# Kernel optimization log

Measured on AMD Instinct MI355X. Metric: run time of the kernel, lower is better.

Reference implementation:

```python
import jax, jax.numpy as jnp
import numpy as np
import math

B, S, D, H = 2, 1024, 4096, 32
HD = D // H          # head_dim = 128
P = 10               # prompt_len
THETA = 500000.0     # rope_theta


def _rope(t, cos, sin):
    # t: [b, s, h, hd]; pairs (2i, 2i+1) form complex numbers as in view_as_complex
    tr = t[..., 0::2]
    ti = t[..., 1::2]
    c = cos[None, :, None, :]
    s = sin[None, :, None, :]
    out = jnp.stack([tr * c - ti * s, tr * s + ti * c], axis=-1)  # [b,s,h,hd/2,2]
    return out.reshape(t.shape)


def setup_inputs() -> dict:
    key = jax.random.key(0)
    ks = jax.random.split(key, 8)
    sc = 0.02
    x = jax.random.normal(ks[0], (B, S, D), jnp.float32)
    wq = jax.random.normal(ks[1], (D, D), jnp.float32) * sc
    wk = jax.random.normal(ks[2], (D, D), jnp.float32) * sc
    wv = jax.random.normal(ks[3], (D, D), jnp.float32) * sc
    wo = jax.random.normal(ks[4], (D, D), jnp.float32) * sc
    prompt = jax.random.normal(ks[5], (P, D), jnp.float32)
    prompt_gate = jax.random.normal(ks[6], (1, H, 1, 1), jnp.float32) * 0.1
    # RoPE tables (real/imag of freqs_cis)
    inv = 1.0 / (THETA ** (jnp.arange(0, HD, 2, dtype=jnp.float32) / HD))  # [HD/2]
    ang = jnp.outer(jnp.arange(S, dtype=jnp.float32), inv)                 # [S, HD/2]
    freqs_cos = jnp.cos(ang)
    freqs_sin = jnp.sin(ang)
    # causal additive mask
    mask = jnp.triu(jnp.full((S, S), -1e9, jnp.float32), 1)[None, None]
    type_weight = jax.random.uniform(ks[7], (B, S, 1), jnp.float32)
    return dict(x=x, wq=wq, wk=wk, wv=wv, wo=wo, prompt=prompt,
                prompt_gate=prompt_gate, freqs_cos=freqs_cos,
                freqs_sin=freqs_sin, mask=mask, type_weight=type_weight,
                start_pos=0)


def reference(x, wq, wk, wv, wo, prompt, prompt_gate, freqs_cos, freqs_sin,
              mask, type_weight, start_pos):
    # training-mode forward: start_pos == 0, keys/values = current tokens
    scale = 1.0 / math.sqrt(HD)
    xq = (x @ wq.T).reshape(B, S, H, HD)
    xk = (x @ wk.T).reshape(B, S, H, HD)
    xv = (x @ wv.T).reshape(B, S, H, HD)
    xq = _rope(xq, freqs_cos, freqs_sin)
    xk = _rope(xk, freqs_cos, freqs_sin)
    q = xq.transpose(0, 2, 1, 3)  # [b,h,s,hd]
    k = xk.transpose(0, 2, 1, 3)
    v = xv.transpose(0, 2, 1, 3)
    scores = jnp.einsum('bhqd,bhkd->bhqk', q, k) * scale + mask
    probs = jax.nn.softmax(scores, axis=-1)
    out = jnp.einsum('bhqk,bhkd->bhqd', probs, v)  # [b,h,s,hd]
    # gated prompt injection (num_experts == 1); type_weight unused, as in source
    pk = (prompt @ wk.T).reshape(P, H, HD)
    pv = (prompt @ wv.T).reshape(P, H, HD)
    p_scores = jnp.einsum('bhqd,phd->bhqp', q, pk) * scale
    p_probs = prompt_gate * jax.nn.softmax(p_scores, axis=-1)
    p_out = jnp.einsum('bhqp,phd->bhqd', p_probs, pv)
    out = (out + p_out).transpose(0, 2, 1, 3).reshape(B, S, D)
    return out @ wo.T
```

## Files before the change

kernel.cpp:

```cpp
#include <hip/hip_runtime.h>
#include <hip/hip_bf16.h>
#include <stdint.h>

typedef __hip_bfloat16 bf16;
typedef __attribute__((ext_vector_type(8))) short short8;
typedef __attribute__((ext_vector_type(4))) float f32x4;

#define SCALE_ 0.08838834764831845f

static __device__ __forceinline__ float bf2f(short u) {
  unsigned int x = ((unsigned int)(unsigned short)u) << 16;
  return __builtin_bit_cast(float, x);
}
static __device__ __forceinline__ short f2bf(float f) {
  __hip_bfloat16 h = __float2bfloat16(f);
  return __builtin_bit_cast(short, h);
}
static __device__ __forceinline__ f32x4 mfma16(short8 a, short8 b, f32x4 c) {
  return __builtin_amdgcn_mfma_f32_16x16x32_bf16(a, b, c, 0, 0, 0);
}
static __device__ __forceinline__ void gl_lds16(const bf16* g, bf16* l) {
  __builtin_amdgcn_global_load_lds(
      (const __attribute__((address_space(1))) unsigned int*)g,
      (__attribute__((address_space(3))) unsigned int*)l, 16, 0, 0);
}

__global__ __launch_bounds__(256) void cvt6(
    const float* __restrict__ sx, const float* __restrict__ sq,
    const float* __restrict__ sk, const float* __restrict__ sv,
    const float* __restrict__ so, const float* __restrict__ sp,
    bf16* __restrict__ dx, bf16* __restrict__ dq, bf16* __restrict__ dk,
    bf16* __restrict__ dv, bf16* __restrict__ d4, bf16* __restrict__ dp)
{
  int b = blockIdx.x;
  const float* s; bf16* d; int off;
  if (b < 4096)       { s = sx; d = dx; off = b; }
  else if (b < 12288) { s = sq; d = dq; off = b - 4096; }
  else if (b < 20480) { s = sk; d = dk; off = b - 12288; }
  else if (b < 28672) { s = sv; d = dv; off = b - 20480; }
  else if (b < 36864) { s = so; d = d4; off = b - 28672; }
  else                { s = sp; d = dp; off = b - 36864; }
  long base = (long)off * 2048 + threadIdx.x * 8;
  f32x4 a = *(const f32x4*)(s + base);
  f32x4 c = *(const f32x4*)(s + base + 4);
  short8 o;
#pragma unroll
  for (int j = 0; j < 4; j++) { o[j] = f2bf(a[j]); o[4 + j] = f2bf(c[j]); }
  *(short8*)(d + base) = o;
}

__global__ __launch_bounds__(512, 2) void gemm_bt(
    const bf16* __restrict__ A, const bf16* __restrict__ A2,
    const bf16* __restrict__ B0, const bf16* __restrict__ B1, const bf16* __restrict__ B2w,
    bf16* __restrict__ C0, bf16* __restrict__ C1, bf16* __restrict__ C2,
    bf16* __restrict__ P1, bf16* __restrict__ P2,
    float* __restrict__ CF,
    int M1, int Mtot)
{
  __shared__ char lds[131072];
  const int tid = threadIdx.x, w = tid >> 6, l = tid & 63;
  const int lr = l & 15, lg = l >> 4;
  const int wm = w >> 2, wn = w & 3;
  const int z = blockIdx.z;
  const bf16* Bw = (z == 0) ? B0 : ((z == 1) ? B1 : B2w);
  bf16* C  = (z == 0) ? C0 : ((z == 1) ? C1 : C2);
  bf16* Cp = (z == 0) ? (bf16*)0 : ((z == 1) ? P1 : P2);

  const int cpx = gridDim.x >> 3, orig = blockIdx.x;
  const int wg = (orig & 7) * cpx + (orig >> 3);
  const long m0 = (long)(wg >> 4) * 256;
  const long n0 = (long)(wg & 15) * 256;

  const int r0 = ((tid >> 3) << 1) | ((tid >> 2) & 1);
  const int c0 = (tid & 3) ^ ((tid >> 3) & 3);
  const bf16 *pa0, *pa1;
  {
    long mx = (long)(Mtot - M1) - 1;
    long g0 = m0 + r0, g1 = m0 + r0 + 128;
    const bf16 *q0, *q1;
    if (g0 < M1) q0 = A + g0 * 4096;
    else { long rr = g0 - M1; if (rr > mx) rr = mx; q0 = A2 + rr * 4096; }
    if (g1 < M1) q1 = A + g1 * 4096;
    else { long rr = g1 - M1; if (rr > mx) rr = mx; q1 = A2 + rr * 4096; }
    pa0 = q0 + c0 * 8;
    pa1 = q1 + c0 * 8;
  }
  const bf16* pb0 = Bw + (n0 + r0) * 4096 + c0 * 8;
  const bf16* pb1 = pb0 + (long)128 * 4096;

  const int ro  = (lr >> 1) * 128 + (((lr & 1) * 4) + (lg ^ ((lr >> 1) & 3))) * 16;
  const int aro = wm * 8192 + ro;
  const int bro = wn * 4096 + ro;

  f32x4 acc[8][4];
#pragma unroll
  for (int i = 0; i < 8; i++)
#pragma unroll
    for (int j = 0; j < 4; j++) acc[i][j] = (f32x4){0.f, 0.f, 0.f, 0.f};

  short8 af[4], bf[4];

#define STG(PSB_, J_, P0_, P1_, KE_)                                         \
  {                                                                          \
    bf16* d_ = (bf16*)(lds + (PSB_) + (J_) * 16384) + tid * 8;               \
    gl_lds16((P0_) + (KE_), d_);                                             \
    gl_lds16((P1_) + (KE_), d_ + 4096);                                      \
  }

#define PHASE(VMS_, PRB_, AU_, BU_, MO_, LB_, STGC_)                         \
  {                                                                          \
    asm volatile("s_waitcnt vmcnt(" VMS_ ")" ::: "memory");                  \
    __builtin_amdgcn_s_barrier();                                            \
    __builtin_amdgcn_sched_barrier(0);                                       \
    STGC_                                                                    \
    const char* ab_ = lds + (PRB_) + (AU_) + aro;                            \
    _Pragma("unroll") for (int mi = 0; mi < 4; mi++)                         \
      af[mi] = *(const short8*)(ab_ + ((MO_) + mi) * 1024);                  \
    if (LB_) {                                                               \
      const char* bb_ = lds + (PRB_) + (BU_) + bro;                          \
      _Pragma("unroll") for (int ni = 0; ni < 4; ni++)                       \
        bf[ni] = *(const short8*)(bb_ + ni * 1024);                          \
    }                                                                        \
    asm volatile("s_waitcnt lgkmcnt(0)" ::: "memory");                       \
    __builtin_amdgcn_sched_barrier(0);                                       \
    __builtin_amdgcn_s_setprio(1);                                           \
    _Pragma("unroll") for (int mi = 0; mi < 4; mi++)                         \
      _Pragma("unroll") for (int ni = 0; ni < 4; ni++)                       \
        acc[(MO_) + mi][ni] = mfma16(af[mi], bf[ni], acc[(MO_) + mi][ni]);   \
    __builtin_amdgcn_s_setprio(0);                                           \
  }

#define KTILE(PRB_, PSB_, KE_)                                               \
  PHASE("4", PRB_, 0,     16384, 0, 1, STG(PSB_, 0, pa0, pa1, (KE_)))        \
  PHASE("4", PRB_, 0,     16384, 4, 0, STG(PSB_, 1, pb0, pb1, (KE_)))        \
  PHASE("4", PRB_, 32768, 49152, 0, 1, STG(PSB_, 2, pa0, pa1, (KE_) + 32))   \
  PHASE("4", PRB_, 32768, 49152, 4, 0, STG(PSB_, 3, pb0, pb1, (KE_) + 32))

#define KTILE_LAST(PRB_)                                                     \
  PHASE("4", PRB_, 0,     16384, 0, 1, )                                     \
  PHASE("4", PRB_, 0,     16384, 4, 0, )                                     \
  PHASE("0", PRB_, 32768, 49152, 0, 1, )                                     \
  PHASE("0", PRB_, 32768, 49152, 4, 0, )

  STG(0, 0, pa0, pa1, 0)
  STG(0, 1, pb0, pb1, 0)
  STG(0, 2, pa0, pa1, 32)
  STG(0, 3, pb0, pb1, 32)

  for (int kt = 0; kt < 62; kt += 2) {
    const int ke1 = (kt + 1) * 64;
    const int ke2 = (kt + 2) * 64;
    KTILE(0, 65536, ke1)
    KTILE(65536, 0, ke2)
  }
  KTILE(0, 65536, 4032)
  KTILE_LAST(65536)

#undef KTILE_LAST
#undef KTILE
#undef PHASE
#undef STG

#pragma unroll
  for (int mi = 0; mi < 8; mi++) {
#pragma unroll
    for (int ni = 0; ni < 4; ni++) {
      long col = n0 + wn * 64 + ni * 16 + lr;
      f32x4 v = acc[mi][ni];
#pragma unroll
      for (int j = 0; j < 4; j++) {
        long row = m0 + wm * 128 + mi * 16 + lg * 4 + j;
        if (CF) {
          CF[row * 4096 + col] = v[j];
        } else if (row < M1) {
          *(short*)(C + row * 4096 + col) = f2bf(v[j]);
        } else if (Cp != 0 && row < Mtot) {
          *(short*)(Cp + (row - M1) * 4096 + col) = f2bf(v[j]);
        }
      }
    }
  }
}

__global__ __launch_bounds__(256) void rope_qk(
    bf16* __restrict__ Q, bf16* __restrict__ Kb,
    const float* __restrict__ FC, const float* __restrict__ FS)
{
  const int row = blockIdx.x;
  const int s = row & 1023;
  const int t = threadIdx.x;
  bf16* base = (blockIdx.y ? Kb : Q) + (long)row * 4096 + t * 16;
  short8 v0 = *(const short8*)base;
  short8 v1 = *(const short8*)(base + 8);
  const float* cp = FC + s * 64 + (t & 7) * 8;
  const float* sp = FS + s * 64 + (t & 7) * 8;
  f32x4 c0 = *(const f32x4*)cp;
  f32x4 c1 = *(const f32x4*)(cp + 4);
  f32x4 s0 = *(const f32x4*)sp;
  f32x4 s1 = *(const f32x4*)(sp + 4);
  short8 o0, o1;
#pragma unroll
  for (int j = 0; j < 4; j++) {
    float c = c0[j], sn = s0[j];
    float e = bf2f(v0[2 * j]), od = bf2f(v0[2 * j + 1]);
    o0[2 * j] = f2bf(e * c - od * sn);
    o0[2 * j + 1] = f2bf(e * sn + od * c);
    float c2 = c1[j], sn2 = s1[j];
    float e2 = bf2f(v1[2 * j]), od2 = bf2f(v1[2 * j + 1]);
    o1[2 * j] = f2bf(e2 * c2 - od2 * sn2);
    o1[2 * j + 1] = f2bf(e2 * sn2 + od2 * c2);
  }
  *(short8*)base = o0;
  *(short8*)(base + 8) = o1;
}

__global__ __launch_bounds__(256) void transpose_v(
    const bf16* __restrict__ V, bf16* __restrict__ VT)
{
  __shared__ bf16 T[64 * 128];
  const int tid = threadIdx.x;
  const int st = blockIdx.x * 64, bh = blockIdx.y;
  const int b = bh >> 5, h = bh & 31;
  const bf16* src = V + ((long)(b * 1024 + st)) * 4096 + h * 128;
#pragma unroll
  for (int rr = 0; rr < 4; ++rr) {
    int i = tid + rr * 256;
    int s_l = i >> 4, c = i & 15;
    short8 v = *(const short8*)(src + (long)s_l * 4096 + c * 8);
    *(short8*)((char*)T + s_l * 256 + ((c ^ (s_l & 7)) * 16)) = v;
  }
  __syncthreads();
#pragma unroll
  for (int rr = 0; rr < 4; ++rr) {
    int i = tid + rr * 256;
    int d = i >> 3, cs = i & 7;
    short8 ov;
#pragma unroll
    for (int e = 0; e < 8; e++) {
      int s_l = cs * 8 + e;
      ov[e] = *(const short*)((char*)T + s_l * 256 + (((d >> 3) ^ (s_l & 7)) * 16) + (d & 7) * 2);
    }
    *(short8*)(VT + ((long)bh * 128 + d) * 1024 + st + cs * 8) = ov;
  }
}

__global__ __launch_bounds__(256) void flash_attn(
    const bf16* __restrict__ Q, const bf16* __restrict__ Kg, const bf16* __restrict__ VT,
    const bf16* __restrict__ PK, const bf16* __restrict__ PV,
    const float* __restrict__ GATE, bf16* __restrict__ O)
{
  __shared__ bf16 Kl[32 * 128];
  __shared__ bf16 Vl[128 * 32];
  __shared__ bf16 PKl[16 * 128];
  __shared__ bf16 PVl[128 * 16];
  __shared__ bf16 Pl[4][16 * 32];
  const int tid = threadIdx.x, w = tid >> 6, l = tid & 63;
  const int lg = l >> 4, lr = l & 15;
  const int qb = blockIdx.x, bh = blockIdx.y;
  const int b = bh >> 5, h = bh & 31;
  const int q0 = qb * 64 + w * 16;

  short8 qf[4];
  {
    const bf16* qp = Q + ((long)(b * 1024 + q0 + lr)) * 4096 + h * 128 + lg * 8;
#pragma unroll
    for (int c = 0; c < 4; c++) qf[c] = *(const short8*)(qp + c * 32);
  }
  {
    int rowp = tid >> 4, pc = tid & 15, lc = pc ^ (rowp & 7);
    short8 v = {0, 0, 0, 0, 0, 0, 0, 0};
    if (rowp < 10) v = *(const short8*)(PK + (long)rowp * 4096 + h * 128 + lc * 8);
    *(short8*)((char*)PKl + tid * 16) = v;
  }
  {
    int d = tid >> 1, pb = (tid & 1) * 8;
#pragma unroll
    for (int e = 0; e < 8; e++) {
      int p = pb + e;
      short v = 0;
      if (p < 10) v = __builtin_bit_cast(short, PV[(long)p * 4096 + h * 128 + d]);
      *(short*)((char*)PVl + d * 32 + (((p >> 3) ^ (d & 1)) * 16) + (p & 7) * 2) = v;
    }
  }
  const float gate = GATE[h];

  f32x4 o[8];
#pragma unroll
  for (int i = 0; i < 8; i++) o[i] = (f32x4){0.f, 0.f, 0.f, 0.f};
  float m_[4] = {-1e30f, -1e30f, -1e30f, -1e30f};
  float l_[4] = {0.f, 0.f, 0.f, 0.f};

  const int nt = (qb + 1) * 2;
  const bf16* Kbase = Kg + ((long)b * 1024) * 4096 + h * 128;
  const bf16* Vbase = VT + ((long)bh) * 128 * 1024;
  const int cb1 = w * 64, cb2 = 256 + w * 64;
  const int iA = cb1 + l, iB = cb2 + l;
  bf16* pw = &Pl[w][0];

  for (int j = 0; j < nt; ++j) {
    __syncthreads();
    {
      const bf16* gA = Kbase + (long)(j * 32 + (iA >> 4)) * 4096 + ((iA & 15) ^ ((iA >> 4) & 7)) * 8;
      const bf16* gB = Kbase + (long)(j * 32 + (iB >> 4)) * 4096 + ((iB & 15) ^ ((iB >> 4) & 7)) * 8;
      gl_lds16(gA, Kl + cb1 * 8);
      gl_lds16(gB, Kl + cb2 * 8);
      const bf16* vA = Vbase + (long)(iA >> 2) * 1024 + j * 32 + ((iA & 3) ^ ((iA >> 2) & 3)) * 8;
      const bf16* vB = Vbase + (long)(iB >> 2) * 1024 + j * 32 + ((iB & 3) ^ ((iB >> 2) & 3)) * 8;
      gl_lds16(vA, Vl + cb1 * 8);
      gl_lds16(vB, Vl + cb2 * 8);
    }
    __syncthreads();

    f32x4 s[2];
#pragma unroll
    for (int ns = 0; ns < 2; ns++) {
      f32x4 a = (f32x4){0.f, 0.f, 0.f, 0.f};
      int krow = ns * 16 + lr;
      const char* kp = (const char*)Kl + krow * 256;
      int sw = krow & 7;
#pragma unroll
      for (int c = 0; c < 4; c++) {
        short8 kf = *(const short8*)(kp + (((c * 4 + lg) ^ sw) * 16));
        a = mfma16(qf[c], kf, a);
      }
      int key = j * 32 + krow;
#pragma unroll
      for (int r = 0; r < 4; r++) {
        int qr = q0 + lg * 4 + r;
        s[ns][r] = a[r] * SCALE_ + ((key <= qr) ? 0.0f : -1e30f);
      }
    }
    float mx[4], cor[4], sum[4];
#pragma unroll
    for (int r = 0; r < 4; r++) mx[r] = fmaxf(s[0][r], s[1][r]);
#pragma unroll
    for (int xm = 1; xm < 16; xm <<= 1)
#pragma unroll
      for (int r = 0; r < 4; r++) mx[r] = fmaxf(mx[r], __shfl_xor(mx[r], xm, 64));
#pragma unroll
    for (int r = 0; r < 4; r++) {
      float mn = fmaxf(m_[r], mx[r]);
      cor[r] = __expf(m_[r] - mn);
      m_[r] = mn;
      s[0][r] = __expf(s[0][r] - mn);
      s[1][r] = __expf(s[1][r] - mn);
      sum[r] = s[0][r] + s[1][r];
    }
#pragma unroll
    for (int xm = 1; xm < 16; xm <<= 1)
#pragma unroll
      for (int r = 0; r < 4; r++) sum[r] += __shfl_xor(sum[r], xm, 64);
#pragma unroll
    for (int r = 0; r < 4; r++) l_[r] = l_[r] * cor[r] + sum[r];
#pragma unroll
    for (int df = 0; df < 8; df++)
#pragma unroll
      for (int r = 0; r < 4; r++) o[df][r] *= cor[r];

#pragma unroll
    for (int ns = 0; ns < 2; ns++)
#pragma unroll
      for (int r = 0; r < 4; r++)
        *(short*)((char*)pw + ((lg * 4 + r) * 32 + ns * 16 + lr) * 2) = f2bf(s[ns][r]);
    asm volatile("s_waitcnt lgkmcnt(0)" ::: "memory");
    __builtin_amdgcn_sched_barrier(0);
    short8 pf = *(const short8*)(pw + lr * 32 + lg * 8);

#pragma unroll
    for (int df = 0; df < 8; df++) {
      int d = df * 16 + lr;
      short8 vf = *(const short8*)((const char*)Vl + d * 64 + ((lg ^ (d & 3)) * 16));
      o[df] = mfma16(pf, vf, o[df]);
    }
  }

  f32x4 ps;
  {
    f32x4 a = (f32x4){0.f, 0.f, 0.f, 0.f};
    const char* kp = (const char*)PKl + lr * 256;
    int sw = lr & 7;
#pragma unroll
    for (int c = 0; c < 4; c++) {
      short8 kf = *(const short8*)(kp + (((c * 4 + lg) ^ sw) * 16));
      a = mfma16(qf[c], kf, a);
    }
#pragma unroll
    for (int r = 0; r < 4; r++) ps[r] = (lr < 10) ? a[r] * SCALE_ : -1e30f;
  }
  {
    float pm[4], pss[4];
#pragma unroll
    for (int r = 0; r < 4; r++) pm[r] = ps[r];
#pragma unroll
    for (int xm = 1; xm < 16; xm <<= 1)
#pragma unroll
      for (int r = 0; r < 4; r++) pm[r] = fmaxf(pm[r], __shfl_xor(pm[r], xm, 64));
#pragma unroll
    for (int r = 0; r < 4; r++) { ps[r] = __expf(ps[r] - pm[r]); pss[r] = ps[r]; }
#pragma unroll
    for (int xm = 1; xm < 16; xm <<= 1)
#pragma unroll
      for (int r = 0; r < 4; r++) pss[r] += __shfl_xor(pss[r], xm, 64);
#pragma unroll
    for (int r = 0; r < 4; r++) ps[r] = ps[r] / pss[r];
  }
#pragma unroll
  for (int r = 0; r < 4; r++) {
    *(short*)((char*)pw + ((lg * 4 + r) * 32 + lr) * 2) = f2bf(ps[r]);
    *(short*)((char*)pw + ((lg * 4 + r) * 32 + 16 + lr) * 2) = 0;
  }
  asm volatile("s_waitcnt lgkmcnt(0)" ::: "memory");
  __builtin_amdgcn_sched_barrier(0);
  short8 pf2 = *(const short8*)(pw + lr * 32 + lg * 8);
  f32x4 po[8];
#pragma unroll
  for (int df = 0; df < 8; df++) {
    int d = df * 16 + lr;
    short8 vf = {0, 0, 0, 0, 0, 0, 0, 0};
    if (lg < 2) vf = *(const short8*)((const char*)PVl + d * 32 + ((lg ^ (d & 1)) * 16));
    po[df] = mfma16(pf2, vf, (f32x4){0.f, 0.f, 0.f, 0.f});
  }

  bf16* op = O + ((long)(b * 1024 + q0 + lg * 4)) * 4096 + h * 128 + lr;
#pragma unroll
  for (int df = 0; df < 8; df++)
#pragma unroll
    for (int r = 0; r < 4; r++) {
      float val = o[df][r] / l_[r] + gate * po[df][r];
      *(short*)(op + (long)r * 4096 + df * 16) = f2bf(val);
    }
}

extern "C" void kernel_launch(void* const* d_in, const int* in_sizes, int n_in,
                              void* d_out, int out_size, void* d_ws, size_t ws_size,
                              hipStream_t stream) {
  (void)in_sizes; (void)n_in; (void)out_size; (void)ws_size;
  const float* x      = (const float*)d_in[0];
  const float* wq     = (const float*)d_in[1];
  const float* wk     = (const float*)d_in[2];
  const float* wv     = (const float*)d_in[3];
  const float* wo     = (const float*)d_in[4];
  const float* prompt = (const float*)d_in[5];
  const float* gate   = (const float*)d_in[6];
  const float* fcos   = (const float*)d_in[7];
  const float* fsin   = (const float*)d_in[8];
  float* out = (float*)d_out;
  char* ws = (char*)d_ws;

  size_t o = 0;
  bf16* xb  = (bf16*)(ws + o); o += (size_t)8388608 * 2;
  bf16* wqb = (bf16*)(ws + o); o += (size_t)16777216 * 2;
  bf16* wkb = (bf16*)(ws + o); o += (size_t)16777216 * 2;
  bf16* wvb = (bf16*)(ws + o); o += (size_t)16777216 * 2;
  bf16* wob = (bf16*)(ws + o); o += (size_t)16777216 * 2;
  bf16* pb  = (bf16*)(ws + o); o += (size_t)40960 * 2;
  bf16* q_ws  = (bf16*)(ws + o); o += (size_t)2048 * 4096 * 2;
  bf16* k_ws  = (bf16*)(ws + o); o += (size_t)2048 * 4096 * 2;
  bf16* v_ws  = (bf16*)(ws + o); o += (size_t)2048 * 4096 * 2;
  bf16* vT_ws = (bf16*)(ws + o); o += (size_t)2048 * 4096 * 2;
  bf16* pk_ws = (bf16*)(ws + o); o += (size_t)40960 * 2;
  bf16* pv_ws = (bf16*)(ws + o); o += (size_t)40960 * 2;
  bf16* attn_ws = v_ws;

  cvt6<<<dim3(36884), 256, 0, stream>>>(x, wq, wk, wv, wo, prompt,
                                        xb, wqb, wkb, wvb, wob, pb);
  gemm_bt<<<dim3(144, 1, 3), 512, 0, stream>>>(
      xb, pb, wqb, wkb, wvb, q_ws, k_ws, v_ws, pk_ws, pv_ws, (float*)0, 2048, 2058);
  rope_qk<<<dim3(2048, 2), 256, 0, stream>>>(q_ws, k_ws, fcos, fsin);
  transpose_v<<<dim3(16, 64), 256, 0, stream>>>(v_ws, vT_ws);
  flash_attn<<<dim3(16, 64), 256, 0, stream>>>(
      q_ws, k_ws, vT_ws, pk_ws, pv_ws, gate, attn_ws);
  gemm_bt<<<dim3(128, 1, 1), 512, 0, stream>>>(
      attn_ws, (const bf16*)0, wob, wob, wob, q_ws, q_ws, q_ws,
      (bf16*)0, (bf16*)0, out, 2048, 2048);
}
```

Before: 530.5 us.

## Deepen GEMM LDS prefetch pipeline and halve barriers per k-tile

Restructures the GEMM main loop so global-to-LDS staging runs further ahead, with six sub-tiles in flight before the first compute instead of four. The eight LDS slots rotate in a new order. Barriers with vmcnt waits now happen once per two phases instead of every phase, which cuts synchronisation stalls. In exchange, each wait tolerates more outstanding loads and the slot reuse is more complex, so there is a risk of LDS read/write races if the slot ordering is wrong.

New measurement: 534.2 us. No clear change (+0.7%).

```diff
diff --git a/kernel.cpp b/kernel.cpp
--- a/kernel.cpp
+++ b/kernel.cpp
@@ -100,19 +100,27 @@
 
   short8 af[4], bf[4];
 
-#define STG(PSB_, J_, P0_, P1_, KE_)                                         \
+#define STGA(S_, KE_)                                                        \
   {                                                                          \
-    bf16* d_ = (bf16*)(lds + (PSB_) + (J_) * 16384) + tid * 8;               \
-    gl_lds16((P0_) + (KE_), d_);                                             \
-    gl_lds16((P1_) + (KE_), d_ + 4096);                                      \
-  }
-
-#define PHASE(VMS_, PRB_, AU_, BU_, MO_, LB_, STGC_)                         \
+    bf16* d_ = (bf16*)(lds + (S_) * 16384) + tid * 8;                        \
+    gl_lds16(pa0 + (KE_), d_);                                               \
+    gl_lds16(pa1 + (KE_), d_ + 4096);                                        \
+  }
+#define STGB(S_, KE_)                                                        \
   {                                                                          \
-    asm volatile("s_waitcnt vmcnt(" VMS_ ")" ::: "memory");                  \
+    bf16* d_ = (bf16*)(lds + (S_) * 16384) + tid * 8;                        \
+    gl_lds16(pb0 + (KE_), d_);                                               \
+    gl_lds16(pb1 + (KE_), d_ + 4096);                                        \
+  }
+#define SYNC(VM_)                                                            \
+  {                                                                          \
+    asm volatile("s_waitcnt vmcnt(" VM_ ")" ::: "memory");                   \
     __builtin_amdgcn_s_barrier();                                            \
     __builtin_amdgcn_sched_barrier(0);                                       \
-    STGC_                                                                    \
+  }
+#define PHASE(PRB_, AU_, BU_, MO_, LB_, STG_)                                \
+  {                                                                          \
+    STG_                                                                     \
     const char* ab_ = lds + (PRB_) + (AU_) + aro;                            \
     _Pragma("unroll") for (int mi = 0; mi < 4; mi++)                         \
       af[mi] = *(const short8*)(ab_ + ((MO_) + mi) * 1024);                  \
@@ -130,36 +138,34 @@
     __builtin_amdgcn_s_setprio(0);                                           \
   }
 
-#define KTILE(PRB_, PSB_, KE_)                                               \
-  PHASE("4", PRB_, 0,     16384, 0, 1, STG(PSB_, 0, pa0, pa1, (KE_)))        \
-  PHASE("4", PRB_, 0,     16384, 4, 0, STG(PSB_, 1, pb0, pb1, (KE_)))        \
-  PHASE("4", PRB_, 32768, 49152, 0, 1, STG(PSB_, 2, pa0, pa1, (KE_) + 32))   \
-  PHASE("4", PRB_, 32768, 49152, 4, 0, STG(PSB_, 3, pb0, pb1, (KE_) + 32))
-
-#define KTILE_LAST(PRB_)                                                     \
-  PHASE("4", PRB_, 0,     16384, 0, 1, )                                     \
-  PHASE("4", PRB_, 0,     16384, 4, 0, )                                     \
-  PHASE("0", PRB_, 32768, 49152, 0, 1, )                                     \
-  PHASE("0", PRB_, 32768, 49152, 4, 0, )
-
-  STG(0, 0, pa0, pa1, 0)
-  STG(0, 1, pb0, pb1, 0)
-  STG(0, 2, pa0, pa1, 32)
-  STG(0, 3, pb0, pb1, 32)
-
-  for (int kt = 0; kt < 62; kt += 2) {
-    const int ke1 = (kt + 1) * 64;
-    const int ke2 = (kt + 2) * 64;
-    KTILE(0, 65536, ke1)
-    KTILE(65536, 0, ke2)
-  }
-  KTILE(0, 65536, 4032)
-  KTILE_LAST(65536)
-
-#undef KTILE_LAST
-#undef KTILE
+#define KT(PRB_, S6_, S7_, S8_, S9_, KE1_, KE2_)                             \
+  SYNC("8") PHASE(PRB_, 0, 16384, 0, 1, STGA(S6_, KE1_))                     \
+  PHASE(PRB_, 0, 16384, 4, 0, STGB(S7_, KE1_))                               \
+  SYNC("8") PHASE(PRB_, 32768, 49152, 0, 1, STGA(S8_, KE2_))                 \
+  PHASE(PRB_, 32768, 49152, 4, 0, STGB(S9_, KE2_))
+
+  STGA(0, 0) STGB(1, 0) STGA(2, 32) STGB(3, 32) STGA(4, 64) STGB(5, 64)
+
+  for (int t = 0; t < 62; t += 2) {
+    const int ka = (t + 1) * 64 + 32, kb = (t + 2) * 64;
+    const int kc = (t + 2) * 64 + 32, kd = (t + 3) * 64;
+    KT(0, 6, 7, 0, 1, ka, kb)
+    KT(65536, 2, 3, 4, 5, kc, kd)
+  }
+  SYNC("8") PHASE(0, 0, 16384, 0, 1, STGA(6, 4064))
+  PHASE(0, 0, 16384, 4, 0, STGB(7, 4064))
+  SYNC("8") PHASE(0, 32768, 49152, 0, 1, )
+  PHASE(0, 32768, 49152, 4, 0, )
+  SYNC("4") PHASE(65536, 0, 16384, 0, 1, )
+  PHASE(65536, 0, 16384, 4, 0, )
+  SYNC("0") PHASE(65536, 32768, 49152, 0, 1, )
+  PHASE(65536, 32768, 49152, 4, 0, )
+
+#undef KT
 #undef PHASE
-#undef STG
+#undef SYNC
+#undef STGB
+#undef STGA
 
 #pragma unroll
   for (int mi = 0; mi < 8; mi++) {
```

## Fuse fp32-to-bf16 conversion into GEMM tile loads, drop separate convert kernel

Applied to the files above, without the earlier changes.

Removes the standalone conversion kernel that rewrote x, all four weight matrices and the prompt to bf16. The GEMM now reads fp32 from global memory into registers, converts to bf16 and writes to LDS with a register-staged pipeline in place of direct global-to-LDS loads. Attention output is also written as fp32 and consumed directly by the output GEMM. This avoids a full extra pass over roughly 270 MB of weights, but the GEMM now streams twice the bytes per tile, uses more registers, and does conversion ALU work in the hot loop, with reuse across the many tiles that read each weight row.

New measurement: 572.9 us. 1.08x slower.

```diff
diff --git a/kernel.cpp b/kernel.cpp
--- a/kernel.cpp
+++ b/kernel.cpp
@@ -25,33 +25,9 @@
       (__attribute__((address_space(3))) unsigned int*)l, 16, 0, 0);
 }
 
-__global__ __launch_bounds__(256) void cvt6(
-    const float* __restrict__ sx, const float* __restrict__ sq,
-    const float* __restrict__ sk, const float* __restrict__ sv,
-    const float* __restrict__ so, const float* __restrict__ sp,
-    bf16* __restrict__ dx, bf16* __restrict__ dq, bf16* __restrict__ dk,
-    bf16* __restrict__ dv, bf16* __restrict__ d4, bf16* __restrict__ dp)
-{
-  int b = blockIdx.x;
-  const float* s; bf16* d; int off;
-  if (b < 4096)       { s = sx; d = dx; off = b; }
-  else if (b < 12288) { s = sq; d = dq; off = b - 4096; }
-  else if (b < 20480) { s = sk; d = dk; off = b - 12288; }
-  else if (b < 28672) { s = sv; d = dv; off = b - 20480; }
-  else if (b < 36864) { s = so; d = d4; off = b - 28672; }
-  else                { s = sp; d = dp; off = b - 36864; }
-  long base = (long)off * 2048 + threadIdx.x * 8;
-  f32x4 a = *(const f32x4*)(s + base);
-  f32x4 c = *(const f32x4*)(s + base + 4);
-  short8 o;
-#pragma unroll
-  for (int j = 0; j < 4; j++) { o[j] = f2bf(a[j]); o[4 + j] = f2bf(c[j]); }
-  *(short8*)(d + base) = o;
-}
-
 __global__ __launch_bounds__(512, 2) void gemm_bt(
-    const bf16* __restrict__ A, const bf16* __restrict__ A2,
-    const bf16* __restrict__ B0, const bf16* __restrict__ B1, const bf16* __restrict__ B2w,
+    const float* __restrict__ A, const float* __restrict__ A2,
+    const float* __restrict__ B0, const float* __restrict__ B1, const float* __restrict__ B2w,
     bf16* __restrict__ C0, bf16* __restrict__ C1, bf16* __restrict__ C2,
     bf16* __restrict__ P1, bf16* __restrict__ P2,
     float* __restrict__ CF,
@@ -62,7 +38,7 @@
   const int lr = l & 15, lg = l >> 4;
   const int wm = w >> 2, wn = w & 3;
   const int z = blockIdx.z;
-  const bf16* Bw = (z == 0) ? B0 : ((z == 1) ? B1 : B2w);
+  const float* Bw = (z == 0) ? B0 : ((z == 1) ? B1 : B2w);
   bf16* C  = (z == 0) ? C0 : ((z == 1) ? C1 : C2);
   bf16* Cp = (z == 0) ? (bf16*)0 : ((z == 1) ? P1 : P2);
 
@@ -73,20 +49,20 @@
 
   const int r0 = ((tid >> 3) << 1) | ((tid >> 2) & 1);
   const int c0 = (tid & 3) ^ ((tid >> 3) & 3);
-  const bf16 *pa0, *pa1;
+  const float *pA0, *pA1;
   {
     long mx = (long)(Mtot - M1) - 1;
     long g0 = m0 + r0, g1 = m0 + r0 + 128;
-    const bf16 *q0, *q1;
+    const float *q0, *q1;
     if (g0 < M1) q0 = A + g0 * 4096;
     else { long rr = g0 - M1; if (rr > mx) rr = mx; q0 = A2 + rr * 4096; }
     if (g1 < M1) q1 = A + g1 * 4096;
     else { long rr = g1 - M1; if (rr > mx) rr = mx; q1 = A2 + rr * 4096; }
-    pa0 = q0 + c0 * 8;
-    pa1 = q1 + c0 * 8;
-  }
-  const bf16* pb0 = Bw + (n0 + r0) * 4096 + c0 * 8;
-  const bf16* pb1 = pb0 + (long)128 * 4096;
+    pA0 = q0 + c0 * 8;
+    pA1 = q1 + c0 * 8;
+  }
+  const float* pB0 = Bw + (n0 + r0) * 4096 + c0 * 8;
+  const float* pB1 = pB0 + (long)128 * 4096;
 
   const int ro  = (lr >> 1) * 128 + (((lr & 1) * 4) + (lg ^ ((lr >> 1) & 3))) * 16;
   const int aro = wm * 8192 + ro;
@@ -99,20 +75,37 @@
     for (int j = 0; j < 4; j++) acc[i][j] = (f32x4){0.f, 0.f, 0.f, 0.f};
 
   short8 af[4], bf[4];
-
-#define STG(PSB_, J_, P0_, P1_, KE_)                                         \
+  f32x4 rgs0[4], rgs1[4], rgs2[4], rgs3[4];
+
+#define LOADU(RG_, ISA_, KE_)                                                \
   {                                                                          \
-    bf16* d_ = (bf16*)(lds + (PSB_) + (J_) * 16384) + tid * 8;               \
-    gl_lds16((P0_) + (KE_), d_);                                             \
-    gl_lds16((P1_) + (KE_), d_ + 4096);                                      \
-  }
-
-#define PHASE(VMS_, PRB_, AU_, BU_, MO_, LB_, STGC_)                         \
+    const float* pl0_ = ((ISA_) ? pA0 : pB0) + (KE_);                        \
+    const float* pl1_ = ((ISA_) ? pA1 : pB1) + (KE_);                        \
+    RG_[0] = *(const f32x4*)pl0_;                                            \
+    RG_[1] = *(const f32x4*)(pl0_ + 4);                                      \
+    RG_[2] = *(const f32x4*)pl1_;                                            \
+    RG_[3] = *(const f32x4*)(pl1_ + 4);                                      \
+  }
+#define WRITEU(RG_, SLB_)                                                    \
   {                                                                          \
-    asm volatile("s_waitcnt vmcnt(" VMS_ ")" ::: "memory");                  \
-    __builtin_amdgcn_s_barrier();                                            \
+    bf16* dw_ = (bf16*)(lds + (SLB_)) + tid * 8;                             \
+    short8 w0_, w1_;                                                         \
+    _Pragma("unroll") for (int q_ = 0; q_ < 4; q_++) {                       \
+      w0_[q_]     = f2bf(RG_[0][q_]); w0_[4 + q_] = f2bf(RG_[1][q_]);        \
+      w1_[q_]     = f2bf(RG_[2][q_]); w1_[4 + q_] = f2bf(RG_[3][q_]);        \
+    }                                                                        \
+    *(short8*)dw_ = w0_;                                                     \
+    *(short8*)(dw_ + 4096) = w1_;                                            \
+  }
+#define VMW(VMS_)                                                            \
+  asm volatile("s_waitcnt vmcnt(" VMS_ ")" ::: "memory");
+#define PHASE(VMS_, BAR_, PRB_, AU_, BU_, MO_, LB_, WC_, LC_)                \
+  {                                                                          \
+    VMW(VMS_)                                                                \
+    BAR_                                                                     \
     __builtin_amdgcn_sched_barrier(0);                                       \
-    STGC_                                                                    \
+    WC_                                                                      \
+    LC_                                                                      \
     const char* ab_ = lds + (PRB_) + (AU_) + aro;                            \
     _Pragma("unroll") for (int mi = 0; mi < 4; mi++)                         \
       af[mi] = *(const short8*)(ab_ + ((MO_) + mi) * 1024);                  \
@@ -129,37 +122,45 @@
         acc[(MO_) + mi][ni] = mfma16(af[mi], bf[ni], acc[(MO_) + mi][ni]);   \
     __builtin_amdgcn_s_setprio(0);                                           \
   }
-
-#define KTILE(PRB_, PSB_, KE_)                                               \
-  PHASE("4", PRB_, 0,     16384, 0, 1, STG(PSB_, 0, pa0, pa1, (KE_)))        \
-  PHASE("4", PRB_, 0,     16384, 4, 0, STG(PSB_, 1, pb0, pb1, (KE_)))        \
-  PHASE("4", PRB_, 32768, 49152, 0, 1, STG(PSB_, 2, pa0, pa1, (KE_) + 32))   \
-  PHASE("4", PRB_, 32768, 49152, 4, 0, STG(PSB_, 3, pb0, pb1, (KE_) + 32))
-
-#define KTILE_LAST(PRB_)                                                     \
-  PHASE("4", PRB_, 0,     16384, 0, 1, )                                     \
-  PHASE("4", PRB_, 0,     16384, 4, 0, )                                     \
-  PHASE("0", PRB_, 32768, 49152, 0, 1, )                                     \
-  PHASE("0", PRB_, 32768, 49152, 4, 0, )
-
-  STG(0, 0, pa0, pa1, 0)
-  STG(0, 1, pb0, pb1, 0)
-  STG(0, 2, pa0, pa1, 32)
-  STG(0, 3, pb0, pb1, 32)
-
-  for (int kt = 0; kt < 62; kt += 2) {
-    const int ke1 = (kt + 1) * 64;
-    const int ke2 = (kt + 2) * 64;
-    KTILE(0, 65536, ke1)
-    KTILE(65536, 0, ke2)
-  }
-  KTILE(0, 65536, 4032)
-  KTILE_LAST(65536)
-
-#undef KTILE_LAST
-#undef KTILE
+#define BARR __builtin_amdgcn_s_barrier();
+
+  LOADU(rgs0, 1, 0)
+  LOADU(rgs1, 0, 0)
+  LOADU(rgs2, 1, 32)
+  LOADU(rgs3, 0, 32)
+  VMW("12") __builtin_amdgcn_sched_barrier(0);
+  WRITEU(rgs0, 0)
+  LOADU(rgs0, 1, 64)
+  VMW("12") __builtin_amdgcn_sched_barrier(0);
+  WRITEU(rgs1, 16384)
+  LOADU(rgs1, 0, 64)
+  asm volatile("s_waitcnt lgkmcnt(0)" ::: "memory");
+  __builtin_amdgcn_sched_barrier(0);
+
+  for (int t = 0; t < 62; ++t) {
+    const int pt = (t & 1) * 65536;
+    const int qt = 65536 - pt;
+    const int keN = (t + 1) * 64 + 32;
+    const int keF = (t + 2) * 64;
+    PHASE("12", BARR, pt, 0,     16384, 0, 1, WRITEU(rgs2, pt + 32768), LOADU(rgs2, 1, keN))
+    PHASE("12",     , pt, 0,     16384, 4, 0, WRITEU(rgs3, pt + 49152), LOADU(rgs3, 0, keN))
+    PHASE("12", BARR, pt, 32768, 49152, 0, 1, WRITEU(rgs0, qt),         LOADU(rgs0, 1, keF))
+    PHASE("12",     , pt, 32768, 49152, 4, 0, WRITEU(rgs1, qt + 16384), LOADU(rgs1, 0, keF))
+  }
+  PHASE("12", BARR, 0, 0,     16384, 0, 1, WRITEU(rgs2, 32768), LOADU(rgs2, 1, 4064))
+  PHASE("12",     , 0, 0,     16384, 4, 0, WRITEU(rgs3, 49152), LOADU(rgs3, 0, 4064))
+  PHASE("12", BARR, 0, 32768, 49152, 0, 1, WRITEU(rgs0, 65536), )
+  PHASE("8",      , 0, 32768, 49152, 4, 0, WRITEU(rgs1, 65536 + 16384), )
+  PHASE("4",  BARR, 65536, 0,     16384, 0, 1, WRITEU(rgs2, 65536 + 32768), )
+  PHASE("0",      , 65536, 0,     16384, 4, 0, WRITEU(rgs3, 65536 + 49152), )
+  PHASE("0",  BARR, 65536, 32768, 49152, 0, 1, , )
+  PHASE("0",      , 65536, 32768, 49152, 4, 0, , )
+
+#undef BARR
 #undef PHASE
-#undef STG
+#undef VMW
+#undef WRITEU
+#undef LOADU
 
 #pragma unroll
   for (int mi = 0; mi < 8; mi++) {
@@ -247,7 +248,7 @@
 __global__ __launch_bounds__(256) void flash_attn(
     const bf16* __restrict__ Q, const bf16* __restrict__ Kg, const bf16* __restrict__ VT,
     const bf16* __restrict__ PK, const bf16* __restrict__ PV,
-    const float* __restrict__ GATE, bf16* __restrict__ O)
+    const float* __restrict__ GATE, float* __restrict__ O)
 {
   __shared__ bf16 Kl[32 * 128];
   __shared__ bf16 Vl[128 * 32];
@@ -421,13 +422,12 @@
     po[df] = mfma16(pf2, vf, (f32x4){0.f, 0.f, 0.f, 0.f});
   }
 
-  bf16* op = O + ((long)(b * 1024 + q0 + lg * 4)) * 4096 + h * 128 + lr;
+  float* op = O + ((long)(b * 1024 + q0 + lg * 4)) * 4096 + h * 128 + lr;
 #pragma unroll
   for (int df = 0; df < 8; df++)
 #pragma unroll
     for (int r = 0; r < 4; r++) {
-      float val = o[df][r] / l_[r] + gate * po[df][r];
-      *(short*)(op + (long)r * 4096 + df * 16) = f2bf(val);
+      op[(long)r * 4096 + df * 16] = o[df][r] / l_[r] + gate * po[df][r];
     }
 }
 
@@ -448,29 +448,21 @@
   char* ws = (char*)d_ws;
 
   size_t o = 0;
-  bf16* xb  = (bf16*)(ws + o); o += (size_t)8388608 * 2;
-  bf16* wqb = (bf16*)(ws + o); o += (size_t)16777216 * 2;
-  bf16* wkb = (bf16*)(ws + o); o += (size_t)16777216 * 2;
-  bf16* wvb = (bf16*)(ws + o); o += (size_t)16777216 * 2;
-  bf16* wob = (bf16*)(ws + o); o += (size_t)16777216 * 2;
-  bf16* pb  = (bf16*)(ws + o); o += (size_t)40960 * 2;
   bf16* q_ws  = (bf16*)(ws + o); o += (size_t)2048 * 4096 * 2;
   bf16* k_ws  = (bf16*)(ws + o); o += (size_t)2048 * 4096 * 2;
   bf16* v_ws  = (bf16*)(ws + o); o += (size_t)2048 * 4096 * 2;
   bf16* vT_ws = (bf16*)(ws + o); o += (size_t)2048 * 4096 * 2;
   bf16* pk_ws = (bf16*)(ws + o); o += (size_t)40960 * 2;
   bf16* pv_ws = (bf16*)(ws + o); o += (size_t)40960 * 2;
-  bf16* attn_ws = v_ws;
-
-  cvt6<<<dim3(36884), 256, 0, stream>>>(x, wq, wk, wv, wo, prompt,
-                                        xb, wqb, wkb, wvb, wob, pb);
+  float* attnF = (float*)(ws + ((o + 255) & ~(size_t)255));
+
   gemm_bt<<<dim3(144, 1, 3), 512, 0, stream>>>(
-      xb, pb, wqb, wkb, wvb, q_ws, k_ws, v_ws, pk_ws, pv_ws, (float*)0, 2048, 2058);
+      x, prompt, wq, wk, wv, q_ws, k_ws, v_ws, pk_ws, pv_ws, (float*)0, 2048, 2058);
   rope_qk<<<dim3(2048, 2), 256, 0, stream>>>(q_ws, k_ws, fcos, fsin);
   transpose_v<<<dim3(16, 64), 256, 0, stream>>>(v_ws, vT_ws);
   flash_attn<<<dim3(16, 64), 256, 0, stream>>>(
-      q_ws, k_ws, vT_ws, pk_ws, pv_ws, gate, attn_ws);
+      q_ws, k_ws, vT_ws, pk_ws, pv_ws, gate, attnF);
   gemm_bt<<<dim3(128, 1, 1), 512, 0, stream>>>(
-      attn_ws, (const bf16*)0, wob, wob, wob, q_ws, q_ws, q_ws,
+      attnF, attnF, wo, wo, wo, q_ws, q_ws, q_ws,
       (bf16*)0, (bf16*)0, out, 2048, 2048);
 }
```
